# Kernel optimization log

Hardware: AMD Instinct MI355X
Metric: run time of the kernel (lower is better)

The kernel has to match this reference:

```python
import jax, jax.numpy as jnp
import numpy as np
import math

D_MODEL = 2048
NUM_HEADS = 16
D_K = D_MODEL // NUM_HEADS  # 128
THETA = 10000.0
BATCH = 2
SEQ = 2048


def setup_inputs() -> dict:
    key = jax.random.key(0)
    k1, k2, k3 = jax.random.split(key, 3)
    std_qkv = math.sqrt(2.0 / (D_MODEL + 3 * D_MODEL))
    std_o = math.sqrt(2.0 / (D_MODEL + D_MODEL))
    return {
        "x": jax.random.normal(k1, (BATCH, SEQ, D_MODEL), dtype=jnp.float32),
        "token_positions": jnp.arange(SEQ, dtype=jnp.int64 if jax.config.jax_enable_x64 else jnp.int32),
        "Wqkv": jax.random.normal(k2, (3 * D_MODEL, D_MODEL), dtype=jnp.float32) * std_qkv,
        "Wo": jax.random.normal(k3, (D_MODEL, D_MODEL), dtype=jnp.float32) * std_o,
    }


def _rope(x, positions):
    # x: [b, h, t, d_k]; interleaved even/odd rotation as in the torch module
    half = D_K // 2
    inv_freq = 1.0 / (THETA ** (jnp.arange(half, dtype=x.dtype) / half))
    ang = positions.astype(x.dtype)[:, None] * inv_freq[None, :]  # [t, half]
    sin, cos = jnp.sin(ang), jnp.cos(ang)                          # broadcast over b,h
    x_even, x_odd = x[..., 0::2], x[..., 1::2]
    rot_even = x_even * cos - x_odd * sin
    rot_odd = x_even * sin + x_odd * cos
    return jnp.stack([rot_even, rot_odd], axis=-1).reshape(x.shape)


def reference(x, token_positions, Wqkv, Wo):
    B, T, _ = x.shape
    qkv = x @ Wqkv.T                                  # [b, t, 3*d_model]
    q, k, v = jnp.split(qkv, 3, axis=-1)
    def to_heads(t):
        return t.reshape(B, T, NUM_HEADS, D_K).transpose(0, 2, 1, 3)  # b h t d
    q, k, v = to_heads(q), to_heads(k), to_heads(v)
    q = _rope(q, token_positions)
    k = _rope(k, token_positions)
    scale = 1.0 / math.sqrt(D_K)
    scores = jnp.einsum("bhqd,bhkd->bhqk", q, k) * scale
    causal = jnp.tril(jnp.ones((T, T), dtype=bool))
    scores = jnp.where(causal, scores, jnp.finfo(scores.dtype).min)
    attn = jax.nn.softmax(scores, axis=-1)
    out = jnp.einsum("bhqk,bhkd->bhqd", attn, v)
    out = out.transpose(0, 2, 1, 3).reshape(B, T, D_MODEL)
    return out @ Wo.T
```

## Files before the change

### kernel.cpp

```cpp
#include <hip/hip_runtime.h>
#include <math.h>
#include <stdint.h>

#define NHEADS 16
#define DK 128
#define TSEQ 2048
#define DMODEL 2048

typedef __attribute__((ext_vector_type(8))) short short8;
typedef __attribute__((ext_vector_type(4))) float floatx4;

__device__ __forceinline__ float bf2f(unsigned short h) {
    return __uint_as_float(((unsigned int)h) << 16);
}
__device__ __forceinline__ unsigned short f2bf(float f) {
    unsigned int u = __float_as_uint(f);
    u += 0x7FFFu + ((u >> 16) & 1u);
    return (unsigned short)(u >> 16);
}
__device__ __forceinline__ void async16(unsigned short* lds, const unsigned short* g) {
    __builtin_amdgcn_global_load_lds(
        (const __attribute__((address_space(1))) uint32_t*)g,
        (__attribute__((address_space(3))) uint32_t*)lds, 16, 0, 0);
}

#define NX8 1048576
#define NW8 1572864
#define NO8 524288
#define NCAST (NX8 + NW8 + NO8)
__global__ __launch_bounds__(256) void cast_rope_kernel(
    const float* __restrict__ x, const float* __restrict__ wqkv, const float* __restrict__ wo,
    const int* __restrict__ pos,
    unsigned short* __restrict__ xb, unsigned short* __restrict__ wqkvb,
    unsigned short* __restrict__ wob, float2* __restrict__ tab)
{
    const int i = blockIdx.x * 256 + threadIdx.x;
    if (i < NCAST) {
        const float* src; unsigned short* dst; int k;
        if (i < NX8)            { src = x;    dst = xb;    k = i; }
        else if (i < NX8 + NW8) { src = wqkv; dst = wqkvb; k = i - NX8; }
        else                    { src = wo;   dst = wob;   k = i - NX8 - NW8; }
        const float4* p4 = reinterpret_cast<const float4*>(src) + 2 * (size_t)k;
        const float4 a = p4[0], b = p4[1];
        uint32_t w0 = (uint32_t)f2bf(a.x) | ((uint32_t)f2bf(a.y) << 16);
        uint32_t w1 = (uint32_t)f2bf(a.z) | ((uint32_t)f2bf(a.w) << 16);
        uint32_t w2 = (uint32_t)f2bf(b.x) | ((uint32_t)f2bf(b.y) << 16);
        uint32_t w3 = (uint32_t)f2bf(b.z) | ((uint32_t)f2bf(b.w) << 16);
        uint4 o; o.x = w0; o.y = w1; o.z = w2; o.w = w3;
        *reinterpret_cast<uint4*>(dst + 8 * (size_t)k) = o;
    } else {
        const int idx = i - NCAST;
        const int tt = idx >> 6, pi = idx & 63;
        const double inv_freq = exp(-log(10000.0) * (double)pi / 64.0);
        const double ang = (double)pos[tt] * inv_freq;
        tab[idx] = make_float2((float)cos(ang), (float)sin(ang));
    }
}

__global__ __launch_bounds__(256, 2) void gemm_qkv_x(
    const unsigned short* __restrict__ A, const unsigned short* __restrict__ B,
    unsigned short* __restrict__ qkvb, unsigned short* __restrict__ vt,
    const float2* __restrict__ tab)
{
    const int K = DMODEL, N = 3 * DMODEL;
    __shared__ unsigned short As[2][128 * 64];
    __shared__ unsigned short Bs[2][192 * 64];

    const int t = threadIdx.x;
    const int lane = t & 63, w = t >> 6;
    const int wr = w >> 1, wc = w & 1;
    const int lr = lane & 15, hi = lane >> 4;

    const int bid = (int)blockIdx.x;
    const int xcd = bid & 7, local = bid >> 3;
    const int row0 = (local & 31) * 128;
    const int col0 = ((xcd << 2) | (local >> 5)) * 192;

    const int rr = t >> 3;
    const int cc = ((t & 7) ^ (rr & 7)) << 3;
    const unsigned short* aP = A + (size_t)(row0 + rr) * K + cc;
    const unsigned short* bP = B + (size_t)(col0 + rr) * K + cc;
    const size_t rstep = (size_t)32 * K;

    floatx4 acc[4][6];
#pragma unroll
    for (int m = 0; m < 4; m++)
#pragma unroll
        for (int n = 0; n < 6; n++)
#pragma unroll
            for (int e = 0; e < 4; e++) acc[m][n][e] = 0.f;

#define STAGE(nb, k0n) do { \
        async16(&As[nb][t * 8],          aP + (k0n)); \
        async16(&As[nb][(t + 256) * 8],  aP + rstep + (k0n)); \
        async16(&As[nb][(t + 512) * 8],  aP + 2 * rstep + (k0n)); \
        async16(&As[nb][(t + 768) * 8],  aP + 3 * rstep + (k0n)); \
        async16(&Bs[nb][t * 8],          bP + (k0n)); \
        async16(&Bs[nb][(t + 256) * 8],  bP + rstep + (k0n)); \
        async16(&Bs[nb][(t + 512) * 8],  bP + 2 * rstep + (k0n)); \
        async16(&Bs[nb][(t + 768) * 8],  bP + 3 * rstep + (k0n)); \
        async16(&Bs[nb][(t + 1024) * 8], bP + 4 * rstep + (k0n)); \
        async16(&Bs[nb][(t + 1280) * 8], bP + 5 * rstep + (k0n)); \
    } while (0)

    const int NT = K >> 6;
    const int ch0 = (hi ^ (lr & 7)) * 8;
    const int ch1 = ((4 + hi) ^ (lr & 7)) * 8;

    short8 av[4], bv[6];

#define RD_AV(Ac, ch) do { \
        _Pragma("unroll") \
        for (int m = 0; m < 4; m++) \
            av[m] = *(const short8*)&(Ac)[(wr * 64 + m * 16 + lr) * 64 + (ch)]; \
    } while (0)
#define RD_BV(Bc, ch) do { \
        _Pragma("unroll") \
        for (int n = 0; n < 6; n++) \
            bv[n] = *(const short8*)&(Bc)[(wc * 96 + n * 16 + lr) * 64 + (ch)]; \
    } while (0)
#define MFMA_ALL() do { \
        _Pragma("unroll") \
        for (int m = 0; m < 4; m++) \
            _Pragma("unroll") \
            for (int n = 0; n < 6; n++) \
                acc[m][n] = __builtin_amdgcn_mfma_f32_16x16x32_bf16(av[m], bv[n], acc[m][n], 0, 0, 0); \
    } while (0)

    STAGE(0, 0);

    for (int kt = 0; kt < NT; ++kt) {
        const int cur = kt & 1;
        const unsigned short* __restrict__ Ac = &As[cur][0];
        const unsigned short* __restrict__ Bc = &Bs[cur][0];
        const bool more = (kt + 1 < NT);

        if (more) {
            STAGE(cur ^ 1, (kt + 1) << 6);
            asm volatile("s_waitcnt vmcnt(10)" ::: "memory");
        } else {
            asm volatile("s_waitcnt vmcnt(0)" ::: "memory");
        }
        __builtin_amdgcn_s_barrier();

        RD_AV(Ac, ch0); RD_BV(Bc, ch0);
        asm volatile("s_waitcnt lgkmcnt(0)" ::: "memory");
        __builtin_amdgcn_sched_barrier(0);
        __builtin_amdgcn_s_setprio(1);
        MFMA_ALL();
        __builtin_amdgcn_s_setprio(0);

        RD_AV(Ac, ch1); RD_BV(Bc, ch1);
        asm volatile("s_waitcnt lgkmcnt(0)" ::: "memory");
        __builtin_amdgcn_sched_barrier(0);
        __builtin_amdgcn_s_setprio(1);
        MFMA_ALL();
        __builtin_amdgcn_s_setprio(0);

        __builtin_amdgcn_s_barrier();
    }
#undef STAGE
#undef RD_AV
#undef RD_BV
#undef MFMA_ALL

    const int par = lr & 1;
#pragma unroll
    for (int mi = 0; mi < 4; mi++) {
        const int row = row0 + wr * 64 + mi * 16 + hi * 4;
        const int tt = row & (TSEQ - 1);
        const int bb = row >> 11;
#pragma unroll
        for (int ni = 0; ni < 6; ni++) {
            const int col = col0 + wc * 96 + ni * 16 + lr;
            if (col < 2 * DMODEL) {
                const int pi = (col & 127) >> 1;
#pragma unroll
                for (int j = 0; j < 4; j++) {
                    const float2 cs = tab[(tt + j) * 64 + pi];
                    const float v = acc[mi][ni][j];
                    const float p = __shfl_xor(v, 1, 64);
                    const float o = par ? (p * cs.y + v * cs.x)
                                        : (v * cs.x - p * cs.y);
                    qkvb[(size_t)(row + j) * N + col] = f2bf(o);
                }
            } else {
                const int vcol = col - 2 * DMODEL;
                const int h = vcol >> 7, d = vcol & 127;
                uint2 pw;
                pw.x = (uint32_t)f2bf(acc[mi][ni][0]) | ((uint32_t)f2bf(acc[mi][ni][1]) << 16);
                pw.y = (uint32_t)f2bf(acc[mi][ni][2]) | ((uint32_t)f2bf(acc[mi][ni][3]) << 16);
                *(uint2*)&vt[(size_t)((bb * NHEADS + h) * DK + d) * TSEQ + tt] = pw;
            }
        }
    }
}

__global__ __launch_bounds__(256, 2) void gemm_o_x(
    const unsigned short* __restrict__ A, const unsigned short* __restrict__ B,
    float* __restrict__ C)
{
    const int K = DMODEL, N = DMODEL;
    __shared__ unsigned short As[2][128 * 64];
    __shared__ unsigned short Bs[2][128 * 64];

    const int t = threadIdx.x;
    const int lane = t & 63, w = t >> 6;
    const int wr = w >> 1, wc = w & 1;
    const int lr = lane & 15, hi = lane >> 4;

    const int bid = (int)blockIdx.x;
    const int xcd = bid & 7, local = bid >> 3;
    const int row0 = (local & 31) * 128;
    const int col0 = ((xcd << 1) | (local >> 5)) * 128;

    const int rr = t >> 3;
    const int cc = ((t & 7) ^ (rr & 7)) << 3;
    const unsigned short* aP = A + (size_t)(row0 + rr) * K + cc;
    const unsigned short* bP = B + (size_t)(col0 + rr) * K + cc;
    const size_t rstep = (size_t)32 * K;

    floatx4 acc[4][4];
#pragma unroll
    for (int m = 0; m < 4; m++)
#pragma unroll
        for (int n = 0; n < 4; n++)
#pragma unroll
            for (int e = 0; e < 4; e++) acc[m][n][e] = 0.f;

#define STAGE(nb, k0n) do { \
        async16(&As[nb][t * 8],          aP + (k0n)); \
        async16(&As[nb][(t + 256) * 8],  aP + rstep + (k0n)); \
        async16(&As[nb][(t + 512) * 8],  aP + 2 * rstep + (k0n)); \
        async16(&As[nb][(t + 768) * 8],  aP + 3 * rstep + (k0n)); \
        async16(&Bs[nb][t * 8],          bP + (k0n)); \
        async16(&Bs[nb][(t + 256) * 8],  bP + rstep + (k0n)); \
        async16(&Bs[nb][(t + 512) * 8],  bP + 2 * rstep + (k0n)); \
        async16(&Bs[nb][(t + 768) * 8],  bP + 3 * rstep + (k0n)); \
    } while (0)

    const int NT = K >> 6;
    const int ch0 = (hi ^ (lr & 7)) * 8;
    const int ch1 = ((4 + hi) ^ (lr & 7)) * 8;

    short8 av[4], bv[4];

#define RD_AV(Ac, ch) do { \
        _Pragma("unroll") \
        for (int m = 0; m < 4; m++) \
            av[m] = *(const short8*)&(Ac)[(wr * 64 + m * 16 + lr) * 64 + (ch)]; \
    } while (0)
#define RD_BV(Bc, ch) do { \
        _Pragma("unroll") \
        for (int n = 0; n < 4; n++) \
            bv[n] = *(const short8*)&(Bc)[(wc * 64 + n * 16 + lr) * 64 + (ch)]; \
    } while (0)
#define MFMA_ALL() do { \
        _Pragma("unroll") \
        for (int m = 0; m < 4; m++) \
            _Pragma("unroll") \
            for (int n = 0; n < 4; n++) \
                acc[m][n] = __builtin_amdgcn_mfma_f32_16x16x32_bf16(av[m], bv[n], acc[m][n], 0, 0, 0); \
    } while (0)

    STAGE(0, 0);

    for (int kt = 0; kt < NT; ++kt) {
        const int cur = kt & 1;
        const unsigned short* __restrict__ Ac = &As[cur][0];
        const unsigned short* __restrict__ Bc = &Bs[cur][0];
        const bool more = (kt + 1 < NT);

        if (more) {
            STAGE(cur ^ 1, (kt + 1) << 6);
            asm volatile("s_waitcnt vmcnt(8)" ::: "memory");
        } else {
            asm volatile("s_waitcnt vmcnt(0)" ::: "memory");
        }
        __builtin_amdgcn_s_barrier();

        RD_AV(Ac, ch0); RD_BV(Bc, ch0);
        asm volatile("s_waitcnt lgkmcnt(0)" ::: "memory");
        __builtin_amdgcn_sched_barrier(0);
        __builtin_amdgcn_s_setprio(1);
        MFMA_ALL();
        __builtin_amdgcn_s_setprio(0);

        RD_AV(Ac, ch1); RD_BV(Bc, ch1);
        asm volatile("s_waitcnt lgkmcnt(0)" ::: "memory");
        __builtin_amdgcn_sched_barrier(0);
        __builtin_amdgcn_s_setprio(1);
        MFMA_ALL();
        __builtin_amdgcn_s_setprio(0);

        __builtin_amdgcn_s_barrier();
    }
#undef STAGE
#undef RD_AV
#undef RD_BV
#undef MFMA_ALL

#pragma unroll
    for (int mi = 0; mi < 4; mi++) {
        const int row = row0 + wr * 64 + mi * 16 + hi * 4;
#pragma unroll
        for (int ni = 0; ni < 4; ni++) {
            const int col = col0 + wc * 64 + ni * 16 + lr;
#pragma unroll
            for (int j = 0; j < 4; j++)
                C[(size_t)(row + j) * N + col] = acc[mi][ni][j];
        }
    }
}

__global__ __launch_bounds__(256, 2) void attn_mfma5_kernel(
    const unsigned short* __restrict__ qkvb, const unsigned short* __restrict__ vt,
    unsigned short* __restrict__ outb)
{
    __shared__ unsigned short Ks[2][64 * 128];
    __shared__ unsigned short Vs[2][128 * 64];
    __shared__ unsigned short Ps[4][32 * 64];

    const int t = threadIdx.x;
    const int lane = t & 63, w = t >> 6;
    const int lr = lane & 15, hi = lane >> 4;
    const int bid  = (int)blockIdx.x;
    const int bh   = bid & 31;
    const int rest = bid >> 5;
    const int p    = rest >> 1;
    const int half = rest & 1;
    const int b = bh >> 4, h = bh & 15;
    const int chunk = (w < 2) ? p : (15 - p);
    const int q0w = chunk * 128 + half * 64 + (w & 1) * 32;
    const float scale = 0.08838834764831845f;
    const size_t QROW = 3 * DMODEL;

    const unsigned short* kg = qkvb + (size_t)b * TSEQ * QROW + DMODEL + h * DK;
    const unsigned short* vg = vt + (size_t)bh * DK * TSEQ;

    short8 qf[2][4];
    {
        const unsigned short* qbase = qkvb + (size_t)(b * TSEQ + q0w) * QROW + h * DK;
#pragma unroll
        for (int nt = 0; nt < 2; nt++)
#pragma unroll
            for (int ks = 0; ks < 4; ks++) {
                short8 raw = *(const short8*)(qbase + (size_t)(nt * 16 + lr) * QROW + ks * 32 + hi * 8);
                short8 sc;
#pragma unroll
                for (int e = 0; e < 8; e++)
                    sc[e] = (short)f2bf(bf2f((unsigned short)raw[e]) * scale);
                qf[nt][ks] = sc;
            }
    }

    auto stageK = [&](int bufi, int kv0s) {
#pragma unroll
        for (int i = 0; i < 4; i++) {
            const int s = i * 256 + t;
            const int r = s >> 4;
            const int cc = (s & 15) ^ (r & 7);
            async16(&Ks[bufi][s * 8], kg + (size_t)(kv0s + r) * QROW + cc * 8);
        }
    };
    auto stageV = [&](int bufi, int kv0s) {
#pragma unroll
        for (int i = 0; i < 4; i++) {
            const int s = i * 256 + t;
            const int r = s >> 3;
            const int cc = (s & 7) ^ (r & 7);
            async16(&Vs[bufi][s * 8], vg + (size_t)r * TSEQ + kv0s + cc * 8);
        }
    };

    floatx4 accO[2][8];
#pragma unroll
    for (int nt = 0; nt < 2; nt++)
#pragma unroll
        for (int dt = 0; dt < 8; dt++)
#pragma unroll
            for (int e = 0; e < 4; e++) accO[nt][dt][e] = 0.f;
    float mrun[2] = {-1e30f, -1e30f};
    float lrun[2] = {0.f, 0.f};

    const int ntiles = (16 - p) * 2;
    int buf = 0;

    stageK(0, 0);
    stageV(0, 0);
    asm volatile("s_waitcnt vmcnt(0)" ::: "memory");
    __builtin_amdgcn_s_barrier();

    const int pswz = (lr & 7) << 1;

    for (int ti = 0; ti < ntiles; ti++) {
        const int kv0 = ti * 64;
        if (ti + 1 < ntiles) {
            stageK(buf ^ 1, kv0 + 64);
            stageV(buf ^ 1, kv0 + 64);
        }

        const bool active = (kv0 <= q0w + 31);

        if (active) {
            float al[2] = {1.f, 1.f};
            floatx4 st[4][2];
#pragma unroll
            for (int mt = 0; mt < 4; mt++)
#pragma unroll
                for (int nt = 0; nt < 2; nt++)
#pragma unroll
                    for (int e = 0; e < 4; e++) st[mt][nt][e] = 0.f;
#pragma unroll
            for (int mt = 0; mt < 4; mt++) {
                const int r = mt * 16 + lr;
#pragma unroll
                for (int ks = 0; ks < 4; ks++) {
                    const int ch = (ks * 4 + hi) ^ (r & 7);
                    const short8 kf = *(const short8*)&Ks[buf][(r * 16 + ch) * 8];
                    st[mt][0] = __builtin_amdgcn_mfma_f32_16x16x32_bf16(kf, qf[0][ks], st[mt][0], 0, 0, 0);
                    st[mt][1] = __builtin_amdgcn_mfma_f32_16x16x32_bf16(kf, qf[1][ks], st[mt][1], 0, 0, 0);
                }
            }
            if (kv0 + 63 > q0w) {
#pragma unroll
                for (int nt = 0; nt < 2; nt++) {
                    const int qg = q0w + nt * 16 + lr;
#pragma unroll
                    for (int mt = 0; mt < 4; mt++)
#pragma unroll
                        for (int rg = 0; rg < 4; rg++) {
                            const int kvg = kv0 + mt * 16 + hi * 4 + rg;
                            if (kvg > qg) st[mt][nt][rg] = -1e30f;
                        }
                }
            }
            float pm[2];
#pragma unroll
            for (int nt = 0; nt < 2; nt++) {
                float m = -1e30f;
#pragma unroll
                for (int mt = 0; mt < 4; mt++)
#pragma unroll
                    for (int rg = 0; rg < 4; rg++) m = fmaxf(m, st[mt][nt][rg]);
                m = fmaxf(m, __shfl_xor(m, 16, 64));
                m = fmaxf(m, __shfl_xor(m, 32, 64));
                pm[nt] = m;
            }
            if (__any((pm[0] > mrun[0] + 8.f) || (pm[1] > mrun[1] + 8.f))) {
#pragma unroll
                for (int nt = 0; nt < 2; nt++) {
                    const float mn = fmaxf(mrun[nt], pm[nt]);
                    al[nt] = __expf(mrun[nt] - mn);
                    mrun[nt] = mn;
                }
#pragma unroll
                for (int rg = 0; rg < 4; rg++) {
                    const float a0 = __shfl(al[0], hi * 4 + rg, 64);
                    const float a1 = __shfl(al[1], hi * 4 + rg, 64);
#pragma unroll
                    for (int dt = 0; dt < 8; dt++) {
                        accO[0][dt][rg] *= a0;
                        accO[1][dt][rg] *= a1;
                    }
                }
            }
#pragma unroll
            for (int nt = 0; nt < 2; nt++) {
                float ls = 0.f;
                const int prow = nt * 16 + lr;
#pragma unroll
                for (int mt = 0; mt < 4; mt++) {
                    float pv[4];
#pragma unroll
                    for (int rg = 0; rg < 4; rg++) {
                        pv[rg] = __expf(st[mt][nt][rg] - mrun[nt]);
                        ls += pv[rg];
                    }
                    uint2 pw;
                    pw.x = (uint32_t)f2bf(pv[0]) | ((uint32_t)f2bf(pv[1]) << 16);
                    pw.y = (uint32_t)f2bf(pv[2]) | ((uint32_t)f2bf(pv[3]) << 16);
                    const int chunkx = (mt * 4 + hi) ^ pswz;
                    *(uint2*)&Ps[w][prow * 64 + chunkx * 4] = pw;
                }
                ls += __shfl_xor(ls, 16, 64);
                ls += __shfl_xor(ls, 32, 64);
                lrun[nt] = lrun[nt] * al[nt] + ls;
            }

#pragma unroll
            for (int ks2 = 0; ks2 < 2; ks2++) {
                const int chp = ((ks2 * 8 + hi * 2) ^ pswz) * 4;
                const short8 pa0 = *(const short8*)&Ps[w][(0 * 16 + lr) * 64 + chp];
                const short8 pa1 = *(const short8*)&Ps[w][(1 * 16 + lr) * 64 + chp];
#pragma unroll
                for (int dt = 0; dt < 8; dt++) {
                    const int r = dt * 16 + lr;
                    const int ch = (ks2 * 4 + hi) ^ (r & 7);
                    const short8 vf = *(const short8*)&Vs[buf][(r * 8 + ch) * 8];
                    accO[0][dt] = __builtin_amdgcn_mfma_f32_16x16x32_bf16(pa0, vf, accO[0][dt], 0, 0, 0);
                    accO[1][dt] = __builtin_amdgcn_mfma_f32_16x16x32_bf16(pa1, vf, accO[1][dt], 0, 0, 0);
                }
            }
        }

        asm volatile("s_waitcnt vmcnt(0)" ::: "memory");
        __builtin_amdgcn_s_barrier();
        buf ^= 1;
    }

#pragma unroll
    for (int nt = 0; nt < 2; nt++) {
        const float lv_own = 1.f / lrun[nt];
#pragma unroll
        for (int rg = 0; rg < 4; rg++) {
            const float lv = __shfl(lv_own, hi * 4 + rg, 64);
            unsigned short* orow = outb + (size_t)(b * TSEQ + q0w + nt * 16 + hi * 4 + rg) * DMODEL + h * DK;
#pragma unroll
            for (int dt = 0; dt < 8; dt++)
                orow[dt * 16 + lr] = f2bf(accO[nt][dt][rg] * lv);
        }
    }
}

extern "C" void kernel_launch(void* const* d_in, const int* in_sizes, int n_in,
                              void* d_out, int out_size, void* d_ws, size_t ws_size,
                              hipStream_t stream)
{
    const float* x    = (const float*)d_in[0];
    const int*   pos  = (const int*)d_in[1];
    const float* Wqkv = (const float*)d_in[2];
    const float* Wo   = (const float*)d_in[3];
    float* out = (float*)d_out;

    unsigned short* qkvb  = (unsigned short*)d_ws;
    unsigned short* vtb   = qkvb + (size_t)25165824;
    unsigned short* xb    = vtb + (size_t)8388608;
    unsigned short* attnb = xb;
    unsigned short* wqkvb = xb + (size_t)8388608;
    unsigned short* wob   = wqkvb + (size_t)12582912;
    float2* tab = (float2*)(wob + (size_t)4194304);

    cast_rope_kernel<<<12800, 256, 0, stream>>>(x, Wqkv, Wo, pos, xb, wqkvb, wob, tab);

    gemm_qkv_x<<<dim3(1024), 256, 0, stream>>>(xb, wqkvb, qkvb, vtb, tab);

    attn_mfma5_kernel<<<dim3(512), 256, 0, stream>>>(qkvb, vtb, attnb);

    gemm_o_x<<<dim3(512), 256, 0, stream>>>(attnb, wob, out);
}
```

Before: 254.8 us.

## Move Wo cast into attention kernel, use exp2 softmax and MFMA priority hints

Takes the Wo fp32-to-bf16 cast out of the first kernel and does it at the start of each attention block, so that work runs inside the attention launch. The softmax now uses base-2 exponentials, with log2(e) folded into the Q scale and the rescale threshold. s_setprio is raised around the two MFMA loops so matrix work gets issue priority over other waves. The extra global traffic at the start of attention can delay its first K/V loads.

```diff
diff --git a/kernel.cpp b/kernel.cpp
--- a/kernel.cpp
+++ b/kernel.cpp
@@ -23,23 +23,25 @@
         (const __attribute__((address_space(1))) uint32_t*)g,
         (__attribute__((address_space(3))) uint32_t*)lds, 16, 0, 0);
 }
+__device__ __forceinline__ float fexp2(float x) {
+    return __builtin_amdgcn_exp2f(x);
+}
 
 #define NX8 1048576
 #define NW8 1572864
 #define NO8 524288
-#define NCAST (NX8 + NW8 + NO8)
+#define NCAST2 (NX8 + NW8)
 __global__ __launch_bounds__(256) void cast_rope_kernel(
-    const float* __restrict__ x, const float* __restrict__ wqkv, const float* __restrict__ wo,
+    const float* __restrict__ x, const float* __restrict__ wqkv,
     const int* __restrict__ pos,
     unsigned short* __restrict__ xb, unsigned short* __restrict__ wqkvb,
-    unsigned short* __restrict__ wob, float2* __restrict__ tab)
+    float2* __restrict__ tab)
 {
     const int i = blockIdx.x * 256 + threadIdx.x;
-    if (i < NCAST) {
+    if (i < NCAST2) {
         const float* src; unsigned short* dst; int k;
-        if (i < NX8)            { src = x;    dst = xb;    k = i; }
-        else if (i < NX8 + NW8) { src = wqkv; dst = wqkvb; k = i - NX8; }
-        else                    { src = wo;   dst = wob;   k = i - NX8 - NW8; }
+        if (i < NX8) { src = x;    dst = xb;    k = i; }
+        else         { src = wqkv; dst = wqkvb; k = i - NX8; }
         const float4* p4 = reinterpret_cast<const float4*>(src) + 2 * (size_t)k;
         const float4 a = p4[0], b = p4[1];
         uint32_t w0 = (uint32_t)f2bf(a.x) | ((uint32_t)f2bf(a.y) << 16);
@@ -49,7 +51,7 @@
         uint4 o; o.x = w0; o.y = w1; o.z = w2; o.w = w3;
         *reinterpret_cast<uint4*>(dst + 8 * (size_t)k) = o;
     } else {
-        const int idx = i - NCAST;
+        const int idx = i - NCAST2;
         const int tt = idx >> 6, pi = idx & 63;
         const double inv_freq = exp(-log(10000.0) * (double)pi / 64.0);
         const double ang = (double)pos[tt] * inv_freq;
@@ -313,9 +315,10 @@
     }
 }
 
-__global__ __launch_bounds__(256, 2) void attn_mfma5_kernel(
+__global__ __launch_bounds__(256, 2) void attn_mfma6_kernel(
     const unsigned short* __restrict__ qkvb, const unsigned short* __restrict__ vt,
-    unsigned short* __restrict__ outb)
+    unsigned short* __restrict__ outb,
+    const float* __restrict__ wo, unsigned short* __restrict__ wob)
 {
     __shared__ unsigned short Ks[2][64 * 128];
     __shared__ unsigned short Vs[2][128 * 64];
@@ -325,6 +328,23 @@
     const int lane = t & 63, w = t >> 6;
     const int lr = lane & 15, hi = lane >> 4;
     const int bid  = (int)blockIdx.x;
+
+    {
+        const int ci = bid * 256 + t;
+#pragma unroll
+        for (int i = 0; i < 4; i++) {
+            const int k = ci + i * 131072;
+            const float4* p4 = reinterpret_cast<const float4*>(wo) + 2 * (size_t)k;
+            const float4 a = p4[0], b = p4[1];
+            uint4 o;
+            o.x = (uint32_t)f2bf(a.x) | ((uint32_t)f2bf(a.y) << 16);
+            o.y = (uint32_t)f2bf(a.z) | ((uint32_t)f2bf(a.w) << 16);
+            o.z = (uint32_t)f2bf(b.x) | ((uint32_t)f2bf(b.y) << 16);
+            o.w = (uint32_t)f2bf(b.z) | ((uint32_t)f2bf(b.w) << 16);
+            *reinterpret_cast<uint4*>(wob + 8 * (size_t)k) = o;
+        }
+    }
+
     const int bh   = bid & 31;
     const int rest = bid >> 5;
     const int p    = rest >> 1;
@@ -332,7 +352,8 @@
     const int b = bh >> 4, h = bh & 15;
     const int chunk = (w < 2) ? p : (15 - p);
     const int q0w = chunk * 128 + half * 64 + (w & 1) * 32;
-    const float scale = 0.08838834764831845f;
+    const float scale2 = 0.08838834764831845f * 1.4426950408889634f;
+    const float THR = 8.f * 1.4426950408889634f;
     const size_t QROW = 3 * DMODEL;
 
     const unsigned short* kg = qkvb + (size_t)b * TSEQ * QROW + DMODEL + h * DK;
@@ -349,7 +370,7 @@
                 short8 sc;
 #pragma unroll
                 for (int e = 0; e < 8; e++)
-                    sc[e] = (short)f2bf(bf2f((unsigned short)raw[e]) * scale);
+                    sc[e] = (short)f2bf(bf2f((unsigned short)raw[e]) * scale2);
                 qf[nt][ks] = sc;
             }
     }
@@ -411,6 +432,7 @@
                 for (int nt = 0; nt < 2; nt++)
 #pragma unroll
                     for (int e = 0; e < 4; e++) st[mt][nt][e] = 0.f;
+            __builtin_amdgcn_s_setprio(1);
 #pragma unroll
             for (int mt = 0; mt < 4; mt++) {
                 const int r = mt * 16 + lr;
@@ -422,6 +444,7 @@
                     st[mt][1] = __builtin_amdgcn_mfma_f32_16x16x32_bf16(kf, qf[1][ks], st[mt][1], 0, 0, 0);
                 }
             }
+            __builtin_amdgcn_s_setprio(0);
             if (kv0 + 63 > q0w) {
 #pragma unroll
                 for (int nt = 0; nt < 2; nt++) {
@@ -447,11 +470,11 @@
                 m = fmaxf(m, __shfl_xor(m, 32, 64));
                 pm[nt] = m;
             }
-            if (__any((pm[0] > mrun[0] + 8.f) || (pm[1] > mrun[1] + 8.f))) {
+            if (__any((pm[0] > mrun[0] + THR) || (pm[1] > mrun[1] + THR))) {
 #pragma unroll
                 for (int nt = 0; nt < 2; nt++) {
                     const float mn = fmaxf(mrun[nt], pm[nt]);
-                    al[nt] = __expf(mrun[nt] - mn);
+                    al[nt] = fexp2(mrun[nt] - mn);
                     mrun[nt] = mn;
                 }
 #pragma unroll
@@ -474,7 +497,7 @@
                     float pv[4];
 #pragma unroll
                     for (int rg = 0; rg < 4; rg++) {
-                        pv[rg] = __expf(st[mt][nt][rg] - mrun[nt]);
+                        pv[rg] = fexp2(st[mt][nt][rg] - mrun[nt]);
                         ls += pv[rg];
                     }
                     uint2 pw;
@@ -488,6 +511,7 @@
                 lrun[nt] = lrun[nt] * al[nt] + ls;
             }
 
+            __builtin_amdgcn_s_setprio(1);
 #pragma unroll
             for (int ks2 = 0; ks2 < 2; ks2++) {
                 const int chp = ((ks2 * 8 + hi * 2) ^ pswz) * 4;
@@ -502,6 +526,7 @@
                     accO[1][dt] = __builtin_amdgcn_mfma_f32_16x16x32_bf16(pa1, vf, accO[1][dt], 0, 0, 0);
                 }
             }
+            __builtin_amdgcn_s_setprio(0);
         }
 
         asm volatile("s_waitcnt vmcnt(0)" ::: "memory");
@@ -541,11 +566,11 @@
     unsigned short* wob   = wqkvb + (size_t)12582912;
     float2* tab = (float2*)(wob + (size_t)4194304);
 
-    cast_rope_kernel<<<12800, 256, 0, stream>>>(x, Wqkv, Wo, pos, xb, wqkvb, wob, tab);
+    cast_rope_kernel<<<10752, 256, 0, stream>>>(x, Wqkv, pos, xb, wqkvb, tab);
 
     gemm_qkv_x<<<dim3(1024), 256, 0, stream>>>(xb, wqkvb, qkvb, vtb, tab);
 
-    attn_mfma5_kernel<<<dim3(512), 256, 0, stream>>>(qkvb, vtb, attnb);
+    attn_mfma6_kernel<<<dim3(512), 256, 0, stream>>>(qkvb, vtb, attnb, Wo, wob);
 
     gemm_o_x<<<dim3(512), 256, 0, stream>>>(attnb, wob, out);
 }
```

Measured after the change: 251.0 us. Within noise of the previous version (-1.5%).
